# Performance work log

Hardware: AMD Instinct MI355X
Metric: run time of the kernel (lower is better)

## Reference

```python
import jax, jax.numpy as jnp
import numpy as np

B = 4096          # batch size
D = 64            # embedding dim
V = 1000000       # num_items
S = 40960         # num_sampled * B = 10 * 4096
NUM_TRIES = 50000 # rejection-sampling tries (deterministic stand-in)


def _sample_unique_log_uniform(rng, num_sampled, num_items):
    """Vectorized stand-in for the torch host-side rejection/dedup loop."""
    ids = np.empty(0, dtype=np.int64)
    while ids.size < num_sampled:
        u = rng.random(num_sampled * 4)
        cand = (np.floor(np.exp(u * np.log(num_items + 1.0))).astype(np.int64) - 1) % num_items
        both = np.concatenate([ids, cand])
        _, first = np.unique(both, return_index=True)
        ids = both[np.sort(first)]  # unique, first-occurrence order
    return ids[:num_sampled]


def setup_inputs() -> dict:
    key = jax.random.key(0)
    k1, k2, k3 = jax.random.split(key, 3)
    rng = np.random.default_rng(0)
    sampled = jnp.asarray(_sample_unique_log_uniform(rng, S, V), dtype=jnp.int64)
    return {
        "user_embeddings": jax.random.normal(k1, (B, D), jnp.float32),
        "item_embeddings": jax.random.normal(k2, (V, D), jnp.float32) * 0.05,
        "item_bias": jnp.zeros((V,), jnp.float32),
        "positive_item_ids": jax.random.randint(k3, (B,), 0, V, dtype=jnp.int64),
        "sampled_item_ids": sampled,
        "num_tries": NUM_TRIES,
    }


def _log_uniform_prob(ids, num_items):
    f = ids.astype(jnp.float32)
    return (jnp.log(f + 2.0) - jnp.log(f + 1.0)) / jnp.log(jnp.float32(num_items + 1))


def _expected_counts(p, num_tries):
    tiny = jnp.float32(np.finfo(np.float32).tiny)
    return jnp.maximum(1.0 - jnp.power(1.0 - p, jnp.float32(num_tries)), tiny)


def reference(user_embeddings, item_embeddings, item_bias, positive_item_ids, sampled_item_ids, num_tries):
    num_items = item_embeddings.shape[0]
    # positive logits [B,1]
    pos_emb = item_embeddings[positive_item_ids]                      # [B,D]
    pos_logits = jnp.sum(user_embeddings * pos_emb, axis=-1, keepdims=True) \
                 + item_bias[positive_item_ids][:, None]
    # sampled logits [B,S]
    samp_emb = item_embeddings[sampled_item_ids]                      # [S,D]
    samp_logits = user_embeddings @ samp_emb.T + item_bias[sampled_item_ids][None, :]
    # mask accidental hits
    hits = positive_item_ids[:, None] == sampled_item_ids[None, :]    # [B,S]
    samp_logits = jnp.where(hits, jnp.float32(-np.finfo(np.float32).max), samp_logits)
    # sampled-softmax expected-count correction
    pos_exp = _expected_counts(_log_uniform_prob(positive_item_ids, num_items), num_tries)
    samp_exp = _expected_counts(_log_uniform_prob(sampled_item_ids, num_items), num_tries)
    pos_logits = pos_logits - jnp.log(pos_exp)[:, None]
    samp_logits = samp_logits - jnp.log(samp_exp)[None, :]
    # cross-entropy with label 0 (the positive column)
    logits = jnp.concatenate([pos_logits, samp_logits], axis=1)       # [B,1+S]
    loss = jnp.mean(jax.nn.logsumexp(logits, axis=-1) - logits[:, 0])
    return loss
```

## Files before the change

### kernel.cpp

```cpp
#include <hip/hip_runtime.h>
#include <math.h>

typedef __attribute__((ext_vector_type(8))) short bf16x8;
typedef __attribute__((ext_vector_type(4))) float f32x4;
typedef __attribute__((ext_vector_type(4))) int i32x4;
typedef __attribute__((ext_vector_type(4))) unsigned short u16x4;

#define LOG2E 1.4426950408889634f
#define LN2   0.6931471805599453f
#define FTINY 1.1754943508222875e-38f
#define MOFF  16.0f

constexpr int Dd = 64;
constexpr int Bb = 4096;
constexpr int Ss = 40960;
constexpr int BN = 256;
constexpr int SCHUNK = 128;
constexpr int STILES = 64;
constexpr int SPB = Ss / STILES;
constexpr int NCHUNK = SPB / SCHUNK;
constexpr int NBLOCKS = STILES * (Bb / BN);
constexpr int IDS_PER_BLOCK = Ss / NBLOCKS;

constexpr int SAMP_BLOCKS = Ss / 16;
constexpr int USER_BLOCKS = (Bb * Dd / 4) / 256;
constexpr int C2_BLOCKS   = Ss / 256;

static __device__ __forceinline__ unsigned short f2bf(float x) {
    unsigned int u = __float_as_uint(x);
    u += 0x7fffu + ((u >> 16) & 1u);
    return (unsigned short)(u >> 16);
}

static __device__ __forceinline__ float neg_log_expected(int id, float invLogV1, float T) {
    float f = (float)id;
    float p = log1pf(1.0f / (f + 1.0f)) * invLogV1;
    float pw = powf(1.0f - p, T);
    float se = fmaxf(1.0f - pw, FTINY);
    return -logf(se);
}

__global__ void k_prep(const float* __restrict__ user, const float* __restrict__ item,
                       const float* __restrict__ bias, const int* __restrict__ sampled,
                       const int* __restrict__ ntries,
                       unsigned short* __restrict__ Ebf, unsigned short* __restrict__ Ubf,
                       float* __restrict__ c2, unsigned int* __restrict__ bm,
                       unsigned int* __restrict__ cnt, float invLogV1, int nbmw, int zb) {
    const int bid = blockIdx.x, tid = threadIdx.x;
    if (bid < SAMP_BLOCKS) {
        const int ri = tid >> 4, c = tid & 15;
        const int s = bid * 16 + ri;
        const int sid = sampled[s];
        f32x4 v = *(const f32x4*)(item + (size_t)sid * Dd + c * 4);
        u16x4 o;
        o[0] = f2bf(v[0]); o[1] = f2bf(v[1]); o[2] = f2bf(v[2]); o[3] = f2bf(v[3]);
        *(u16x4*)(Ebf + (size_t)s * Dd + c * 4) = o;
    } else if (bid < SAMP_BLOCKS + zb) {
        const int z = bid - SAMP_BLOCKS;
        if (z == 0 && tid == 0) *cnt = 0u;
        const int base = (z * 256 + tid) * 4;
        if (base + 3 < nbmw) {
            i32x4 zz = {0, 0, 0, 0};
            *(i32x4*)((int*)bm + base) = zz;
        } else {
            for (int i = base; i < nbmw; ++i) bm[i] = 0u;
        }
    } else if (bid < SAMP_BLOCKS + zb + USER_BLOCKS) {
        const int i = (bid - SAMP_BLOCKS - zb) * 256 + tid;
        f32x4 v = *(const f32x4*)(user + (size_t)i * 4);
        u16x4 o;
        o[0] = f2bf(v[0] * LOG2E); o[1] = f2bf(v[1] * LOG2E);
        o[2] = f2bf(v[2] * LOG2E); o[3] = f2bf(v[3] * LOG2E);
        *(u16x4*)(Ubf + (size_t)i * 4) = o;
    } else {
        const int s = (bid - SAMP_BLOCKS - zb - USER_BLOCKS) * 256 + tid;
        const int sid = sampled[s];
        const float T = (float)ntries[0];
        c2[s] = (bias[sid] + neg_log_expected(sid, invLogV1, T)) * LOG2E - MOFF;
    }
}

__global__ __launch_bounds__(256) void ssl_main(
    const unsigned short* __restrict__ Ebf, const unsigned short* __restrict__ Ubf,
    const float* __restrict__ c2, const int* __restrict__ sampled,
    unsigned int* __restrict__ bm, float* __restrict__ partials)
{
    __shared__ __align__(16) unsigned short lds[SCHUNK * Dd];
    const int tid = threadIdx.x;
    const int w = tid >> 6, l = tid & 63;
    const int g16 = l >> 4, l16 = l & 15;
    const int stile = blockIdx.x, btile = blockIdx.y;

    const int fid = stile + STILES * btile;
    if (tid < IDS_PER_BLOCK) {
        const int sid = sampled[fid * IDS_PER_BLOCK + tid];
        atomicOr(&bm[sid >> 5], 1u << (sid & 31));
    }

    const int s0 = stile * SPB;
    const int colb = btile * BN + w * 64;
    bf16x8 bf[4][2];
    #pragma unroll
    for (int g = 0; g < 4; ++g) {
        const unsigned short* up = Ubf + (size_t)(colb + g * 16 + l16) * Dd + g16 * 8;
        bf[g][0] = *(const bf16x8*)(up);
        bf[g][1] = *(const bf16x8*)(up + 32);
    }

    float rl0 = 0.f, rl1 = 0.f, rl2 = 0.f, rl3 = 0.f;

    const int srow = tid >> 3, scs = tid & 7;
    const int csrc = scs ^ (srow & 7);
    const unsigned short* stgp = Ebf + (size_t)(s0 + srow) * Dd + csrc * 8;
    bf16x8 stg0 = *(const bf16x8*)(stgp);
    bf16x8 stg1 = *(const bf16x8*)(stgp + 32 * Dd);
    bf16x8 stg2 = *(const bf16x8*)(stgp + 64 * Dd);
    bf16x8 stg3 = *(const bf16x8*)(stgp + 96 * Dd);
    const float* c2b = c2 + s0 + g16 * 4;

    for (int ch = 0; ch < NCHUNK; ++ch) {
        __syncthreads();
        *(bf16x8*)(lds + tid * 8)           = stg0;
        *(bf16x8*)(lds + tid * 8 + 32 * Dd) = stg1;
        *(bf16x8*)(lds + tid * 8 + 64 * Dd) = stg2;
        *(bf16x8*)(lds + tid * 8 + 96 * Dd) = stg3;
        if (ch + 1 < NCHUNK) {
            const unsigned short* np = stgp + (size_t)(ch + 1) * SCHUNK * Dd;
            stg0 = *(const bf16x8*)(np);
            stg1 = *(const bf16x8*)(np + 32 * Dd);
            stg2 = *(const bf16x8*)(np + 64 * Dd);
            stg3 = *(const bf16x8*)(np + 96 * Dd);
        }
        __syncthreads();

        const float* c2c = c2b + ch * SCHUNK;
        #pragma unroll
        for (int t = 0; t < 8; ++t) {
            const int r = t * 16 + l16;
            const int sw = r & 7;
            const bf16x8 a0 = *(const bf16x8*)(lds + r * Dd + (((g16    ) ^ sw) << 3));
            const bf16x8 a1 = *(const bf16x8*)(lds + r * Dd + (((g16 + 4) ^ sw) << 3));
            const f32x4 cc = *(const f32x4*)(c2c + t * 16);
            #pragma unroll
            for (int g = 0; g < 4; ++g) {
                f32x4 acc = __builtin_amdgcn_mfma_f32_16x16x32_bf16(a0, bf[g][0], cc, 0, 0, 0);
                acc = __builtin_amdgcn_mfma_f32_16x16x32_bf16(a1, bf[g][1], acc, 0, 0, 0);
                float e = (__builtin_amdgcn_exp2f(acc[0]) + __builtin_amdgcn_exp2f(acc[1]))
                        + (__builtin_amdgcn_exp2f(acc[2]) + __builtin_amdgcn_exp2f(acc[3]));
                if      (g == 0) rl0 += e;
                else if (g == 1) rl1 += e;
                else if (g == 2) rl2 += e;
                else             rl3 += e;
            }
        }
    }

    rl0 += __shfl_xor(rl0, 16); rl0 += __shfl_xor(rl0, 32);
    rl1 += __shfl_xor(rl1, 16); rl1 += __shfl_xor(rl1, 32);
    rl2 += __shfl_xor(rl2, 16); rl2 += __shfl_xor(rl2, 32);
    rl3 += __shfl_xor(rl3, 16); rl3 += __shfl_xor(rl3, 32);
    if (l < 16) {
        partials[(size_t)(colb +  0 + l16) * STILES + stile] = rl0;
        partials[(size_t)(colb + 16 + l16) * STILES + stile] = rl1;
        partials[(size_t)(colb + 32 + l16) * STILES + stile] = rl2;
        partials[(size_t)(colb + 48 + l16) * STILES + stile] = rl3;
    }
}

__global__ void k_final(const float* __restrict__ user, const float* __restrict__ item,
                        const float* __restrict__ bias, const int* __restrict__ posids,
                        const int* __restrict__ ntries, const float* __restrict__ partials,
                        const unsigned int* __restrict__ bm,
                        float* __restrict__ bsums, unsigned int* __restrict__ cnt,
                        float* __restrict__ out, float invLogV1) {
    const int tid = threadIdx.x, sub = tid & 3;
    const int b = blockIdx.x * 64 + (tid >> 2);
    const int pid = posids[b];
    const float T = (float)ntries[0];
    const f32x4* up = (const f32x4*)(user + (size_t)b * Dd + sub * 16);
    const f32x4* ep = (const f32x4*)(item + (size_t)pid * Dd + sub * 16);
    f32x4 dv = {0.f, 0.f, 0.f, 0.f};
    #pragma unroll
    for (int i = 0; i < 4; ++i) {
        f32x4 uu = up[i], ee = ep[i];
        dv[0] = fmaf(uu[0], ee[0], dv[0]); dv[1] = fmaf(uu[1], ee[1], dv[1]);
        dv[2] = fmaf(uu[2], ee[2], dv[2]); dv[3] = fmaf(uu[3], ee[3], dv[3]);
    }
    float d = (dv[0] + dv[1]) + (dv[2] + dv[3]);
    d += __shfl_xor(d, 1); d += __shfl_xor(d, 2);
    const float* pp = partials + (size_t)b * STILES + sub * 16;
    float S = 0.f;
    #pragma unroll
    for (int i = 0; i < 4; ++i) {
        f32x4 pv = *(const f32x4*)(pp + i * 4);
        S += ((pv[0] + pv[1]) + (pv[2] + pv[3]));
    }
    S += __shfl_xor(S, 1); S += __shfl_xor(S, 2);

    const float pb2 = (d + bias[pid] + neg_log_expected(pid, invLogV1, T)) * LOG2E;
    const bool hit = (bm[pid >> 5] >> (pid & 31)) & 1u;
    if (!hit) S += __builtin_amdgcn_exp2f(pb2 - MOFF);
    float loss = (MOFF + log2f(S) - pb2) * LN2;

    #pragma unroll
    for (int off = 1; off < 64; off <<= 1) loss += __shfl_xor(loss, off);
    __shared__ float wsum[4];
    if ((tid & 63) == 0) wsum[tid >> 6] = loss;
    __syncthreads();
    if (tid == 0) {
        bsums[blockIdx.x] = wsum[0] + wsum[1] + wsum[2] + wsum[3];
        __threadfence();
        if (atomicAdd(cnt, 1u) == 63u) {
            __threadfence();
            float tot = 0.f;
            for (int i = 0; i < 64; ++i) tot += bsums[i];
            out[0] = tot * (1.0f / (4.0f * (float)Bb));
        }
    }
}

extern "C" void kernel_launch(void* const* d_in, const int* in_sizes, int n_in,
                              void* d_out, int out_size, void* d_ws, size_t ws_size,
                              hipStream_t stream) {
    (void)n_in; (void)out_size; (void)ws_size;
    const float* user    = (const float*)d_in[0];
    const float* item    = (const float*)d_in[1];
    const float* bias    = (const float*)d_in[2];
    const int*   posids  = (const int*)d_in[3];
    const int*   sampled = (const int*)d_in[4];
    const int*   ntries  = (const int*)d_in[5];
    float* out = (float*)d_out;

    const int V = in_sizes[2];
    const float invLogV1 = 1.0f / logf((float)V + 1.0f);
    const int nbmw = (V + 31) / 32;
    const int zb = (nbmw + 1023) / 1024;

    char* p = (char*)d_ws;
    auto alloc = [&](size_t bytes) {
        char* r = p;
        p += (bytes + 255) & ~(size_t)255;
        return r;
    };
    unsigned short* Ebf     = (unsigned short*)alloc((size_t)Ss * Dd * 2);
    unsigned short* Ubf     = (unsigned short*)alloc((size_t)Bb * Dd * 2);
    float*          c2      = (float*)alloc((size_t)Ss * 4);
    float*          partial = (float*)alloc((size_t)Bb * STILES * 4);
    unsigned int*   bm      = (unsigned int*)alloc((size_t)nbmw * 4);
    float*          bsums   = (float*)alloc(64 * 4);
    unsigned int*   cnt     = (unsigned int*)alloc(256);

    k_prep<<<SAMP_BLOCKS + zb + USER_BLOCKS + C2_BLOCKS, 256, 0, stream>>>(
        user, item, bias, sampled, ntries, Ebf, Ubf, c2, bm, cnt, invLogV1, nbmw, zb);
    ssl_main<<<dim3(STILES, Bb / BN), 256, 0, stream>>>(Ebf, Ubf, c2, sampled, bm, partial);
    k_final<<<Bb / 64, 256, 0, stream>>>(user, item, bias, posids, ntries,
                                         partial, bm, bsums, cnt, out, invLogV1);
}
```

Measured before the change: 52.61 us.

## Double-buffer sampled-embedding chunks in LDS with direct global-to-LDS loads

Replaces register staging of each 128-row embedding chunk with `global_load_lds` DMA writes straight into a two-slot LDS buffer. The next chunk now loads while the current one is consumed by MFMAs, and one of the two barriers per chunk goes away. The bias/correction vectors for a chunk are also loaded into registers up front. The cost is double the LDS footprint and a correctness dependence on the barrier waiting for outstanding vector-memory loads before the buffer is read.

```diff
diff --git a/kernel.cpp b/kernel.cpp
--- a/kernel.cpp
+++ b/kernel.cpp
@@ -30,6 +30,13 @@
     unsigned int u = __float_as_uint(x);
     u += 0x7fffu + ((u >> 16) & 1u);
     return (unsigned short)(u >> 16);
+}
+
+static __device__ __forceinline__ void gload16(const unsigned short* g, unsigned short* l) {
+    __builtin_amdgcn_global_load_lds(
+        (const __attribute__((address_space(1))) unsigned int*)g,
+        (__attribute__((address_space(3))) unsigned int*)l,
+        16, 0, 0);
 }
 
 static __device__ __forceinline__ float neg_log_expected(int id, float invLogV1, float T) {
@@ -85,7 +92,7 @@
     const float* __restrict__ c2, const int* __restrict__ sampled,
     unsigned int* __restrict__ bm, float* __restrict__ partials)
 {
-    __shared__ __align__(16) unsigned short lds[SCHUNK * Dd];
+    __shared__ __align__(16) unsigned short lds[2][SCHUNK * Dd];
     const int tid = threadIdx.x;
     const int w = tid >> 6, l = tid & 63;
     const int g16 = l >> 4, l16 = l & 15;
@@ -112,35 +119,41 @@
     const int srow = tid >> 3, scs = tid & 7;
     const int csrc = scs ^ (srow & 7);
     const unsigned short* stgp = Ebf + (size_t)(s0 + srow) * Dd + csrc * 8;
-    bf16x8 stg0 = *(const bf16x8*)(stgp);
-    bf16x8 stg1 = *(const bf16x8*)(stgp + 32 * Dd);
-    bf16x8 stg2 = *(const bf16x8*)(stgp + 64 * Dd);
-    bf16x8 stg3 = *(const bf16x8*)(stgp + 96 * Dd);
     const float* c2b = c2 + s0 + g16 * 4;
+
+    {
+        const unsigned short* g0 = stgp;
+        unsigned short* lb = &lds[0][tid * 8];
+        gload16(g0,            lb);
+        gload16(g0 + 32 * Dd,  lb + 32 * Dd);
+        gload16(g0 + 64 * Dd,  lb + 64 * Dd);
+        gload16(g0 + 96 * Dd,  lb + 96 * Dd);
+    }
 
     for (int ch = 0; ch < NCHUNK; ++ch) {
         __syncthreads();
-        *(bf16x8*)(lds + tid * 8)           = stg0;
-        *(bf16x8*)(lds + tid * 8 + 32 * Dd) = stg1;
-        *(bf16x8*)(lds + tid * 8 + 64 * Dd) = stg2;
-        *(bf16x8*)(lds + tid * 8 + 96 * Dd) = stg3;
         if (ch + 1 < NCHUNK) {
             const unsigned short* np = stgp + (size_t)(ch + 1) * SCHUNK * Dd;
-            stg0 = *(const bf16x8*)(np);
-            stg1 = *(const bf16x8*)(np + 32 * Dd);
-            stg2 = *(const bf16x8*)(np + 64 * Dd);
-            stg3 = *(const bf16x8*)(np + 96 * Dd);
-        }
-        __syncthreads();
+            unsigned short* lb = &lds[(ch + 1) & 1][tid * 8];
+            gload16(np,            lb);
+            gload16(np + 32 * Dd,  lb + 32 * Dd);
+            gload16(np + 64 * Dd,  lb + 64 * Dd);
+            gload16(np + 96 * Dd,  lb + 96 * Dd);
+        }
 
         const float* c2c = c2b + ch * SCHUNK;
+        f32x4 ccv[8];
+        #pragma unroll
+        for (int t = 0; t < 8; ++t) ccv[t] = *(const f32x4*)(c2c + t * 16);
+
+        const unsigned short* ldsb = lds[ch & 1];
         #pragma unroll
         for (int t = 0; t < 8; ++t) {
             const int r = t * 16 + l16;
             const int sw = r & 7;
-            const bf16x8 a0 = *(const bf16x8*)(lds + r * Dd + (((g16    ) ^ sw) << 3));
-            const bf16x8 a1 = *(const bf16x8*)(lds + r * Dd + (((g16 + 4) ^ sw) << 3));
-            const f32x4 cc = *(const f32x4*)(c2c + t * 16);
+            const bf16x8 a0 = *(const bf16x8*)(ldsb + r * Dd + (((g16    ) ^ sw) << 3));
+            const bf16x8 a1 = *(const bf16x8*)(ldsb + r * Dd + (((g16 + 4) ^ sw) << 3));
+            const f32x4 cc = ccv[t];
             #pragma unroll
             for (int g = 0; g < 4; ++g) {
                 f32x4 acc = __builtin_amdgcn_mfma_f32_16x16x32_bf16(a0, bf[g][0], cc, 0, 0, 0);
```

New measurement: 64.63 us. 22.9% more time.
